# Kernel tuning notes

Measured on AMD Instinct MI355X. Metric: run time of the kernel, lower is better.

The kernel has to match this reference:

```python
import jax, jax.numpy as jnp
from jax import lax
import numpy as np

B, T, F, H, L = 256, 512, 64, 128, 2


def lstm_layer(x, W_ih, W_hh, b_ih, b_hh):
    """PyTorch-style LSTM layer. x:[B,T,I]; W_ih:[4H,I]; W_hh:[4H,H]. Gate order i,f,g,o."""
    b = x.shape[0]
    h_dim = W_hh.shape[1]
    # Precompute input contribution for all timesteps: [B,T,4H]
    xg = jnp.einsum('bti,gi->btg', x, W_ih) + b_ih + b_hh

    def step(carry, xg_t):
        h, c = carry
        g = xg_t + h @ W_hh.T  # [B,4H]
        i, f, gg, o = jnp.split(g, 4, axis=-1)
        c = jax.nn.sigmoid(f) * c + jax.nn.sigmoid(i) * jnp.tanh(gg)
        h = jax.nn.sigmoid(o) * jnp.tanh(c)
        return (h, c), h

    h0 = jnp.zeros((b, h_dim), x.dtype)
    c0 = jnp.zeros((b, h_dim), x.dtype)
    (hT, _), hs = lax.scan(step, (h0, c0), jnp.swapaxes(xg, 0, 1))  # hs:[T,B,H]
    return jnp.swapaxes(hs, 0, 1), hT


def setup_inputs() -> dict:
    key = jax.random.key(0)
    ks = iter(jax.random.split(key, 32))
    s = 0.05
    d = {"x": jax.random.normal(next(ks), (B, T, F), jnp.float32)}
    # encoder: layer0 input F, layer1 input H; decoder: both layers input H
    for name, in0 in (("enc", F), ("dec", H)):
        for l in range(L):
            I = in0 if l == 0 else H
            d[f"{name}{l}_Wih"] = jax.random.normal(next(ks), (4 * H, I), jnp.float32) * s
            d[f"{name}{l}_Whh"] = jax.random.normal(next(ks), (4 * H, H), jnp.float32) * s
            d[f"{name}{l}_bih"] = jax.random.normal(next(ks), (4 * H,), jnp.float32) * s
            d[f"{name}{l}_bhh"] = jax.random.normal(next(ks), (4 * H,), jnp.float32) * s
    d["W_out"] = jax.random.normal(next(ks), (F, H), jnp.float32) * s
    d["b_out"] = jnp.zeros((F,), jnp.float32)
    return d


def reference(x,
              enc0_Wih, enc0_Whh, enc0_bih, enc0_bhh,
              enc1_Wih, enc1_Whh, enc1_bih, enc1_bhh,
              dec0_Wih, dec0_Whh, dec0_bih, dec0_bhh,
              dec1_Wih, dec1_Whh, dec1_bih, dec1_bhh,
              W_out, b_out):
    enc = [(enc0_Wih, enc0_Whh, enc0_bih, enc0_bhh),
           (enc1_Wih, enc1_Whh, enc1_bih, enc1_bhh)]
    dec = [(dec0_Wih, dec0_Whh, dec0_bih, dec0_bhh),
           (dec1_Wih, dec1_Whh, dec1_bih, dec1_bhh)]
    # Encoder: stacked LSTM, keep last layer's final hidden state
    h = x
    hT = None
    for p in enc:
        h, hT = lstm_layer(h, *p)
    # Repeat final hidden over sequence
    dec_in = jnp.broadcast_to(hT[:, None, :], (x.shape[0], x.shape[1], hT.shape[-1]))
    # Decoder: stacked LSTM over full output sequence
    d = dec_in
    for p in dec:
        d, _ = lstm_layer(d, *p)
    # Linear projection back to feature space
    return jnp.einsum('bth,fh->btf', d, W_out) + b_out
```

## Files before the change

kernel.cpp:

```cpp
#include <hip/hip_runtime.h>
#include <cstddef>

namespace {

typedef _Float16 half_t;
typedef _Float16 half2_t __attribute__((ext_vector_type(2)));
typedef _Float16 f16x4 __attribute__((ext_vector_type(4)));
typedef _Float16 f16x8 __attribute__((ext_vector_type(8)));
typedef float f32x4 __attribute__((ext_vector_type(4)));

constexpr int NB = 256;
constexpr int NT = 512;
constexpr int NH = 128;
constexpr int NG = 512;

__device__ __forceinline__ float sigm(float x) { return 1.0f / (1.0f + __expf(-x)); }
__device__ __forceinline__ float tanh_(float x) { return 2.0f / (1.0f + __expf(-2.0f * x)) - 1.0f; }
__device__ __forceinline__ float dot4(float4 w, float4 v, float acc) {
  return fmaf(w.x, v.x, fmaf(w.y, v.y, fmaf(w.z, v.z, fmaf(w.w, v.w, acc))));
}
__device__ __forceinline__ float fdot2(half2_t a, half2_t b, float c) {
  return __builtin_amdgcn_fdot2(a, b, c, false);
}
__device__ __forceinline__ void pinv(half2_t& x) { asm volatile("" : "+v"(x)); }

__global__ void cvt_kernel(const float* __restrict__ s, half_t* __restrict__ d, int n4) {
  int i = blockIdx.x * blockDim.x + threadIdx.x;
  if (i < n4) {
    float4 v = reinterpret_cast<const float4*>(s)[i];
    f16x4 hv = {(half_t)v.x, (half_t)v.y, (half_t)v.z, (half_t)v.w};
    reinterpret_cast<f16x4*>(d)[i] = hv;
  }
}

template <int K, bool AF32, bool F32OUT>
__global__ __launch_bounds__(256) void xg_gemm(
    const void* __restrict__ Ap, const float* __restrict__ Bw,
    const float* __restrict__ b0, const float* __restrict__ b1,
    half_t* __restrict__ Ch, float* __restrict__ Cf, int Nstr)
{
  __shared__ __align__(16) half_t Atile[128 * K];
  __shared__ __align__(16) half_t Btile[64 * K];
  const int tid = threadIdx.x;
  const int m0 = blockIdx.x * 128;
  const int n0 = blockIdx.y * 64;
  char* Ab = (char*)Atile;
  char* Bb = (char*)Btile;

  if (AF32) {
    const float* Af = (const float*)Ap;
    for (int idx = tid; idx < 128 * K / 4; idx += 256) {
      int row = idx / (K / 4), o = idx % (K / 4);
      float4 v = *(const float4*)(Af + (size_t)(m0 + row) * K + 4 * o);
      f16x4 hv = {(half_t)v.x, (half_t)v.y, (half_t)v.z, (half_t)v.w};
      int byte = ((row * K + 4 * o) * 2) ^ ((row & 7) << 4);
      *(f16x4*)(Ab + byte) = hv;
    }
  } else {
    const half_t* Ah = (const half_t*)Ap;
    for (int idx = tid; idx < 128 * K / 8; idx += 256) {
      int row = idx / (K / 8), o = idx % (K / 8);
      uint4 v = *(const uint4*)(Ah + (size_t)(m0 + row) * K + 8 * o);
      int byte = ((row * K + 8 * o) * 2) ^ ((row & 7) << 4);
      *(uint4*)(Ab + byte) = v;
    }
  }
  for (int idx = tid; idx < 64 * K / 4; idx += 256) {
    int row = idx / (K / 4), o = idx % (K / 4);
    float4 v = *(const float4*)(Bw + (size_t)(n0 + row) * K + 4 * o);
    f16x4 hv = {(half_t)v.x, (half_t)v.y, (half_t)v.z, (half_t)v.w};
    int byte = ((row * K + 4 * o) * 2) ^ ((row & 7) << 4);
    *(f16x4*)(Bb + byte) = hv;
  }
  __syncthreads();

  const int lane = tid & 63, w = tid >> 6;
  const int r16 = lane & 15, koff = (lane >> 4) * 8;
  f32x4 acc[2][4];
#pragma unroll
  for (int fm = 0; fm < 2; ++fm)
#pragma unroll
    for (int fn = 0; fn < 4; ++fn) acc[fm][fn] = (f32x4){0.f, 0.f, 0.f, 0.f};

#pragma unroll
  for (int ks = 0; ks < K / 32; ++ks) {
    f16x8 a[2], bf[4];
#pragma unroll
    for (int fm = 0; fm < 2; ++fm) {
      int row = w * 32 + fm * 16 + r16;
      int byte = ((row * K + ks * 32 + koff) * 2) ^ ((row & 7) << 4);
      a[fm] = *(const f16x8*)(Ab + byte);
    }
#pragma unroll
    for (int fn = 0; fn < 4; ++fn) {
      int row = fn * 16 + r16;
      int byte = ((row * K + ks * 32 + koff) * 2) ^ ((row & 7) << 4);
      bf[fn] = *(const f16x8*)(Bb + byte);
    }
#pragma unroll
    for (int fm = 0; fm < 2; ++fm)
#pragma unroll
      for (int fn = 0; fn < 4; ++fn)
        acc[fm][fn] = __builtin_amdgcn_mfma_f32_16x16x32_f16(a[fm], bf[fn], acc[fm][fn], 0, 0, 0);
  }

#pragma unroll
  for (int fm = 0; fm < 2; ++fm)
#pragma unroll
    for (int fn = 0; fn < 4; ++fn) {
      int n = n0 + fn * 16 + r16;
      float bb = (b0 ? b0[n] : 0.f) + (b1 ? b1[n] : 0.f);
#pragma unroll
      for (int q = 0; q < 4; ++q) {
        int m = m0 + w * 32 + fm * 16 + (lane >> 4) * 4 + q;
        float val = acc[fm][fn][q] + bb;
        if (F32OUT) Cf[(size_t)m * Nstr + n] = val;
        else        Ch[(size_t)m * Nstr + n] = (half_t)val;
      }
    }
}

template <int MODE>
__global__ __launch_bounds__(512, 2) void rec_kernel(
    const half_t* __restrict__ xg,
    const float* __restrict__ hT_in,
    const float* __restrict__ WihD,
    const float* __restrict__ bih, const float* __restrict__ bhh,
    const half_t* __restrict__ Whh,
    half_t* __restrict__ seq_out,
    float* __restrict__ hT_out)
{
  const int b = blockIdx.x;
  const int tid = threadIdx.x;
  const int j = tid >> 2;
  const int kq = tid & 3;

  __shared__ __align__(16) half_t hbuf[2][4][48];
  __shared__ __align__(16) half_t xgs[2][8][NG];
  __shared__ float xgc[NG];
  __shared__ float hinf[NH];

  half2_t wh[4][16];
#pragma unroll
  for (int gi = 0; gi < 4; ++gi) {
    const half2_t* p = reinterpret_cast<const half2_t*>(Whh + (size_t)(gi * NH + j) * NH + kq * 32);
#pragma unroll
    for (int r = 0; r < 16; ++r) wh[gi][r] = p[r];
  }
#pragma unroll
  for (int gi = 0; gi < 4; ++gi)
#pragma unroll
    for (int r = 0; r < 16; ++r) pinv(wh[gi][r]);

  if (tid < NH) hbuf[0][tid >> 5][tid & 31] = (half_t)0.0f;
  float c = 0.0f;

  if (MODE == 2) {
    if (tid < NH) hinf[tid] = hT_in[(size_t)b * NH + tid];
    __syncthreads();
    float a0 = bih[tid] + bhh[tid], a1 = 0.f, a2 = 0.f, a3 = 0.f;
    const float4* wr = (const float4*)(WihD + (size_t)tid * NH);
    const float4* hv = (const float4*)hinf;
#pragma unroll
    for (int k = 0; k < 8; ++k) {
      a0 = dot4(wr[4 * k + 0], hv[4 * k + 0], a0);
      a1 = dot4(wr[4 * k + 1], hv[4 * k + 1], a1);
      a2 = dot4(wr[4 * k + 2], hv[4 * k + 2], a2);
      a3 = dot4(wr[4 * k + 3], hv[4 * k + 3], a3);
    }
    xgc[tid] = (a0 + a1) + (a2 + a3);
    __syncthreads();
  }

  half_t g[8];
  const half_t* xrow = nullptr;
  if (MODE != 2) {
    xrow = xg + (size_t)b * NT * NG + tid;
#pragma unroll
    for (int s = 0; s < 8; ++s) g[s] = xrow[(size_t)s * NG];
  }

  for (int ch = 0; ch < NT / 8; ++ch) {
    if (MODE != 2) {
#pragma unroll
      for (int s = 0; s < 8; ++s) xgs[ch & 1][s][tid] = g[s];
      if (ch < NT / 8 - 1) {
#pragma unroll
        for (int s = 0; s < 8; ++s) g[s] = xrow[(size_t)((ch + 1) * 8 + s) * NG];
      }
      __syncthreads();
    }

#pragma unroll 1
    for (int tt = 0; tt < 8; ++tt) {
      const int t = ch * 8 + tt;
      const int p = t & 1;

      float a0 = 0.f, a1 = 0.f, a2 = 0.f, a3 = 0.f;
      const f16x8* hv8 = reinterpret_cast<const f16x8*>(&hbuf[p][kq][0]);
#pragma unroll
      for (int r8 = 0; r8 < 4; ++r8) {
        f16x8 h8 = hv8[r8];
        half2_t h0 = {h8[0], h8[1]}, h1 = {h8[2], h8[3]};
        half2_t h2 = {h8[4], h8[5]}, h3 = {h8[6], h8[7]};
        a0 = fdot2(wh[0][4 * r8 + 0], h0, a0); a0 = fdot2(wh[0][4 * r8 + 1], h1, a0);
        a0 = fdot2(wh[0][4 * r8 + 2], h2, a0); a0 = fdot2(wh[0][4 * r8 + 3], h3, a0);
        a1 = fdot2(wh[1][4 * r8 + 0], h0, a1); a1 = fdot2(wh[1][4 * r8 + 1], h1, a1);
        a1 = fdot2(wh[1][4 * r8 + 2], h2, a1); a1 = fdot2(wh[1][4 * r8 + 3], h3, a1);
        a2 = fdot2(wh[2][4 * r8 + 0], h0, a2); a2 = fdot2(wh[2][4 * r8 + 1], h1, a2);
        a2 = fdot2(wh[2][4 * r8 + 2], h2, a2); a2 = fdot2(wh[2][4 * r8 + 3], h3, a2);
        a3 = fdot2(wh[3][4 * r8 + 0], h0, a3); a3 = fdot2(wh[3][4 * r8 + 1], h1, a3);
        a3 = fdot2(wh[3][4 * r8 + 2], h2, a3); a3 = fdot2(wh[3][4 * r8 + 3], h3, a3);
      }
      a0 += __shfl_xor(a0, 1, 4); a0 += __shfl_xor(a0, 2, 4);
      a1 += __shfl_xor(a1, 1, 4); a1 += __shfl_xor(a1, 2, 4);
      a2 += __shfl_xor(a2, 1, 4); a2 += __shfl_xor(a2, 2, 4);
      a3 += __shfl_xor(a3, 1, 4); a3 += __shfl_xor(a3, 2, 4);

      float xi, xf, xgg, xo;
      if (MODE == 2) {
        xi = xgc[j]; xf = xgc[j + 128]; xgg = xgc[j + 256]; xo = xgc[j + 384];
      } else {
        const half_t* xb = &xgs[ch & 1][tt][0];
        xi = (float)xb[j]; xf = (float)xb[j + 128];
        xgg = (float)xb[j + 256]; xo = (float)xb[j + 384];
      }

      const float ig = sigm(a0 + xi);
      const float fg = sigm(a1 + xf);
      const float gg = tanh_(a2 + xgg);
      const float og = sigm(a3 + xo);
      c = fmaf(fg, c, ig * gg);
      const float h = og * tanh_(c);

      if (kq == 0) {
        hbuf[p ^ 1][j >> 5][j & 31] = (half_t)h;
        if (MODE != 1) seq_out[((size_t)b * NT + t) * NH + j] = (half_t)h;
        else if (t == NT - 1) hT_out[(size_t)b * NH + j] = h;
      }
      __syncthreads();
    }
  }
}

}

extern "C" void kernel_launch(void* const* d_in, const int* in_sizes, int n_in,
                              void* d_out, int out_size, void* d_ws, size_t ws_size,
                              hipStream_t stream) {
  (void)in_sizes; (void)n_in; (void)out_size; (void)ws_size;

  const float* x     = (const float*)d_in[0];
  const float* e0Wih = (const float*)d_in[1];
  const float* e0Whh = (const float*)d_in[2];
  const float* e0bih = (const float*)d_in[3];
  const float* e0bhh = (const float*)d_in[4];
  const float* e1Wih = (const float*)d_in[5];
  const float* e1Whh = (const float*)d_in[6];
  const float* e1bih = (const float*)d_in[7];
  const float* e1bhh = (const float*)d_in[8];
  const float* d0Wih = (const float*)d_in[9];
  const float* d0Whh = (const float*)d_in[10];
  const float* d0bih = (const float*)d_in[11];
  const float* d0bhh = (const float*)d_in[12];
  const float* d1Wih = (const float*)d_in[13];
  const float* d1Whh = (const float*)d_in[14];
  const float* d1bih = (const float*)d_in[15];
  const float* d1bhh = (const float*)d_in[16];
  const float* Wout  = (const float*)d_in[17];
  const float* bout  = (const float*)d_in[18];
  float* out = (float*)d_out;

  half_t* whh0 = (half_t*)d_ws;
  half_t* whh1 = whh0 + 512 * 128;
  half_t* whh2 = whh1 + 512 * 128;
  half_t* whh3 = whh2 + 512 * 128;
  half_t* seqA = whh3 + 512 * 128;
  half_t* xgb  = seqA + (size_t)NB * NT * NH;
  float*  hT   = (float*)(xgb + (size_t)NB * NT * NG);

  cvt_kernel<<<64, 256, 0, stream>>>(e0Whh, whh0, 512 * 128 / 4);
  cvt_kernel<<<64, 256, 0, stream>>>(e1Whh, whh1, 512 * 128 / 4);
  cvt_kernel<<<64, 256, 0, stream>>>(d0Whh, whh2, 512 * 128 / 4);
  cvt_kernel<<<64, 256, 0, stream>>>(d1Whh, whh3, 512 * 128 / 4);

  const int M = NB * NT;
  dim3 gX(M / 128, NG / 64), gP(M / 128, 1), blkG(256);
  dim3 gR(NB), blkR(512);

  xg_gemm<64, true, false><<<gX, blkG, 0, stream>>>(x, e0Wih, e0bih, e0bhh, xgb, nullptr, NG);
  rec_kernel<0><<<gR, blkR, 0, stream>>>(xgb, nullptr, nullptr, nullptr, nullptr, whh0, seqA, nullptr);

  xg_gemm<128, false, false><<<gX, blkG, 0, stream>>>(seqA, e1Wih, e1bih, e1bhh, xgb, nullptr, NG);
  rec_kernel<1><<<gR, blkR, 0, stream>>>(xgb, nullptr, nullptr, nullptr, nullptr, whh1, nullptr, hT);

  rec_kernel<2><<<gR, blkR, 0, stream>>>(nullptr, hT, d0Wih, d0bih, d0bhh, whh2, seqA, nullptr);

  xg_gemm<128, false, false><<<gX, blkG, 0, stream>>>(seqA, d1Wih, d1bih, d1bhh, xgb, nullptr, NG);
  rec_kernel<0><<<gR, blkR, 0, stream>>>(xgb, nullptr, nullptr, nullptr, nullptr, whh3, seqA, nullptr);

  xg_gemm<128, false, true><<<gP, blkG, 0, stream>>>(seqA, Wout, bout, nullptr, nullptr, out, 64);
}
```

Before: 1.984 ms.

## Batch 16 sequences per block and compute LSTM recurrence with MFMA

The recurrent kernel now processes 16 batch rows per block (16 blocks instead of 256) and computes h@W_hh^T with 16x16x32 f16 MFMA instructions, with W_hh held in registers as MFMA fragments. The input-gate GEMM writes its output in a time-major, fragment-tiled layout so each lane loads its gate preactivations directly, prefetched two steps ahead. Hidden states are staged in an 8-deep shared-memory ring and flushed to a time-major sequence buffer every 8 steps. The intent is to replace per-row scalar dot2 math and shuffle reductions with matrix instructions, at the cost of using only 16 workgroups on a large GPU and serial per-step latency per block.

Result: slower. 3.575 ms (+80.2%).

```diff
diff --git a/kernel.cpp b/kernel.cpp
--- a/kernel.cpp
+++ b/kernel.cpp
@@ -4,7 +4,6 @@
 namespace {
 
 typedef _Float16 half_t;
-typedef _Float16 half2_t __attribute__((ext_vector_type(2)));
 typedef _Float16 f16x4 __attribute__((ext_vector_type(4)));
 typedef _Float16 f16x8 __attribute__((ext_vector_type(8)));
 typedef float f32x4 __attribute__((ext_vector_type(4)));
@@ -16,13 +15,11 @@
 
 __device__ __forceinline__ float sigm(float x) { return 1.0f / (1.0f + __expf(-x)); }
 __device__ __forceinline__ float tanh_(float x) { return 2.0f / (1.0f + __expf(-2.0f * x)) - 1.0f; }
-__device__ __forceinline__ float dot4(float4 w, float4 v, float acc) {
-  return fmaf(w.x, v.x, fmaf(w.y, v.y, fmaf(w.z, v.z, fmaf(w.w, v.w, acc))));
-}
-__device__ __forceinline__ float fdot2(half2_t a, half2_t b, float c) {
-  return __builtin_amdgcn_fdot2(a, b, c, false);
-}
-__device__ __forceinline__ void pinv(half2_t& x) { asm volatile("" : "+v"(x)); }
+__device__ __forceinline__ void pinv8(f16x8& x) { asm volatile("" : "+v"(x)); }
+
+__device__ __forceinline__ size_t xg_off(int t, int bblk, int w, int fn, int u, int row) {
+  return ((size_t)((t * 16 + bblk) * 8 + w)) * 1024 + (size_t)((fn * 16 + u) * 16 + row);
+}
 
 __global__ void cvt_kernel(const float* __restrict__ s, half_t* __restrict__ d, int n4) {
   int i = blockIdx.x * blockDim.x + threadIdx.x;
@@ -33,11 +30,11 @@
   }
 }
 
-template <int K, bool AF32, bool F32OUT>
+template <int K, int AMAP, int OUT>
 __global__ __launch_bounds__(256) void xg_gemm(
     const void* __restrict__ Ap, const float* __restrict__ Bw,
     const float* __restrict__ b0, const float* __restrict__ b1,
-    half_t* __restrict__ Ch, float* __restrict__ Cf, int Nstr)
+    half_t* __restrict__ Co, float* __restrict__ Cf)
 {
   __shared__ __align__(16) half_t Atile[128 * K];
   __shared__ __align__(16) half_t Btile[64 * K];
@@ -47,11 +44,12 @@
   char* Ab = (char*)Atile;
   char* Bb = (char*)Btile;
 
-  if (AF32) {
+  if (AMAP == 1) {
     const float* Af = (const float*)Ap;
+    const int t_fix = m0 >> 8, b_base = m0 & 255;
     for (int idx = tid; idx < 128 * K / 4; idx += 256) {
       int row = idx / (K / 4), o = idx % (K / 4);
-      float4 v = *(const float4*)(Af + (size_t)(m0 + row) * K + 4 * o);
+      float4 v = *(const float4*)(Af + ((size_t)(b_base + row) * NT + t_fix) * K + 4 * o);
       f16x4 hv = {(half_t)v.x, (half_t)v.y, (half_t)v.z, (half_t)v.w};
       int byte = ((row * K + 4 * o) * 2) ^ ((row & 7) << 4);
       *(f16x4*)(Ab + byte) = hv;
@@ -74,8 +72,8 @@
   }
   __syncthreads();
 
-  const int lane = tid & 63, w = tid >> 6;
-  const int r16 = lane & 15, koff = (lane >> 4) * 8;
+  const int lane = tid & 63, wv = tid >> 6;
+  const int r16 = lane & 15, g4 = lane >> 4, koff = g4 * 8;
   f32x4 acc[2][4];
 #pragma unroll
   for (int fm = 0; fm < 2; ++fm)
@@ -87,7 +85,7 @@
     f16x8 a[2], bf[4];
 #pragma unroll
     for (int fm = 0; fm < 2; ++fm) {
-      int row = w * 32 + fm * 16 + r16;
+      int row = wv * 32 + fm * 16 + r16;
       int byte = ((row * K + ks * 32 + koff) * 2) ^ ((row & 7) << 4);
       a[fm] = *(const f16x8*)(Ab + byte);
     }
@@ -104,142 +102,176 @@
         acc[fm][fn] = __builtin_amdgcn_mfma_f32_16x16x32_f16(a[fm], bf[fn], acc[fm][fn], 0, 0, 0);
   }
 
-#pragma unroll
-  for (int fm = 0; fm < 2; ++fm)
-#pragma unroll
-    for (int fn = 0; fn < 4; ++fn) {
-      int n = n0 + fn * 16 + r16;
-      float bb = (b0 ? b0[n] : 0.f) + (b1 ? b1[n] : 0.f);
-#pragma unroll
-      for (int q = 0; q < 4; ++q) {
-        int m = m0 + w * 32 + fm * 16 + (lane >> 4) * 4 + q;
-        float val = acc[fm][fn][q] + bb;
-        if (F32OUT) Cf[(size_t)m * Nstr + n] = val;
-        else        Ch[(size_t)m * Nstr + n] = (half_t)val;
-      }
-    }
+  if (OUT == 0) {
+    const int t = m0 >> 8;
+#pragma unroll
+    for (int fm = 0; fm < 2; ++fm)
+#pragma unroll
+      for (int fn = 0; fn < 4; ++fn) {
+        const int gate = n0 + fn * 16 + r16;
+        const float bb = b0[gate] + b1[gate];
+        const int b_lo = (m0 & 255) + wv * 32 + fm * 16 + g4 * 4;
+        const int bblk = b_lo >> 4, row = b_lo & 15;
+        const int fnG = gate >> 7, w2 = (gate & 127) >> 4;
+        const size_t off =
+            ((size_t)(t * 16 + bblk) * 8 + w2) * 1024 + (size_t)((fnG * 16 + r16) * 16 + row);
+        f16x4 pk = {(half_t)(acc[fm][fn][0] + bb), (half_t)(acc[fm][fn][1] + bb),
+                    (half_t)(acc[fm][fn][2] + bb), (half_t)(acc[fm][fn][3] + bb)};
+        *(f16x4*)(Co + off) = pk;
+      }
+  } else {
+    const int t = m0 >> 8;
+#pragma unroll
+    for (int fm = 0; fm < 2; ++fm)
+#pragma unroll
+      for (int fn = 0; fn < 4; ++fn) {
+        const int n = n0 + fn * 16 + r16;
+        const float bb = b0[n];
+#pragma unroll
+        for (int q = 0; q < 4; ++q) {
+          const int b = (m0 & 255) + wv * 32 + fm * 16 + g4 * 4 + q;
+          Cf[((size_t)b * NT + t) * 64 + n] = acc[fm][fn][q] + bb;
+        }
+      }
+  }
 }
 
 template <int MODE>
-__global__ __launch_bounds__(512, 2) void rec_kernel(
-    const half_t* __restrict__ xg,
-    const float* __restrict__ hT_in,
-    const float* __restrict__ WihD,
+__global__ __attribute__((amdgpu_flat_work_group_size(512, 512)))
+__attribute__((amdgpu_waves_per_eu(2, 2))) void rec_mfma(
+    const half_t* __restrict__ xgF,
+    const float* __restrict__ hT_in, const float* __restrict__ Wih32,
     const float* __restrict__ bih, const float* __restrict__ bhh,
     const half_t* __restrict__ Whh,
     half_t* __restrict__ seq_out,
     float* __restrict__ hT_out)
 {
-  const int b = blockIdx.x;
   const int tid = threadIdx.x;
-  const int j = tid >> 2;
-  const int kq = tid & 3;
-
-  __shared__ __align__(16) half_t hbuf[2][4][48];
-  __shared__ __align__(16) half_t xgs[2][8][NG];
-  __shared__ float xgc[NG];
-  __shared__ float hinf[NH];
-
-  half2_t wh[4][16];
-#pragma unroll
-  for (int gi = 0; gi < 4; ++gi) {
-    const half2_t* p = reinterpret_cast<const half2_t*>(Whh + (size_t)(gi * NH + j) * NH + kq * 32);
-#pragma unroll
-    for (int r = 0; r < 16; ++r) wh[gi][r] = p[r];
-  }
-#pragma unroll
-  for (int gi = 0; gi < 4; ++gi)
-#pragma unroll
-    for (int r = 0; r < 16; ++r) pinv(wh[gi][r]);
-
-  if (tid < NH) hbuf[0][tid >> 5][tid & 31] = (half_t)0.0f;
-  float c = 0.0f;
-
+  const int w = tid >> 6, lane = tid & 63;
+  const int u = lane & 15, g4 = lane >> 4;
+  const int bblk = blockIdx.x, b0 = bblk * 16;
+
+  __shared__ __align__(16) half_t hist[8][16][136];
+
+  f16x8 wh[4][4];
+#pragma unroll
+  for (int fn = 0; fn < 4; ++fn)
+#pragma unroll
+    for (int ks = 0; ks < 4; ++ks)
+      wh[fn][ks] =
+          *(const f16x8*)(Whh + (size_t)(fn * 128 + w * 16 + u) * NH + ks * 32 + g4 * 8);
+#pragma unroll
+  for (int fn = 0; fn < 4; ++fn)
+#pragma unroll
+    for (int ks = 0; ks < 4; ++ks) pinv8(wh[fn][ks]);
+
+  {
+    int m = tid >> 5, k0 = (tid & 31) * 4;
+    f16x4 z = {(half_t)0.f, (half_t)0.f, (half_t)0.f, (half_t)0.f};
+    *(f16x4*)&hist[7][m][k0] = z;
+  }
+
+  float c[4] = {0.f, 0.f, 0.f, 0.f};
+
+  f32x4 accC[4];
   if (MODE == 2) {
-    if (tid < NH) hinf[tid] = hT_in[(size_t)b * NH + tid];
+    f16x8 ah[4];
+#pragma unroll
+    for (int ks = 0; ks < 4; ++ks) {
+      const float* hp = hT_in + (size_t)(b0 + u) * NH + ks * 32 + g4 * 8;
+      float4 v0 = *(const float4*)hp, v1 = *(const float4*)(hp + 4);
+      f16x8 t8;
+      t8[0] = (half_t)v0.x; t8[1] = (half_t)v0.y; t8[2] = (half_t)v0.z; t8[3] = (half_t)v0.w;
+      t8[4] = (half_t)v1.x; t8[5] = (half_t)v1.y; t8[6] = (half_t)v1.z; t8[7] = (half_t)v1.w;
+      ah[ks] = t8;
+    }
+#pragma unroll
+    for (int fn = 0; fn < 4; ++fn) {
+      const int gate = fn * 128 + w * 16 + u;
+      f32x4 a = {0.f, 0.f, 0.f, 0.f};
+#pragma unroll
+      for (int ks = 0; ks < 4; ++ks) {
+        const float* wp = Wih32 + (size_t)gate * NH + ks * 32 + g4 * 8;
+        float4 v0 = *(const float4*)wp, v1 = *(const float4*)(wp + 4);
+        f16x8 t8;
+        t8[0] = (half_t)v0.x; t8[1] = (half_t)v0.y; t8[2] = (half_t)v0.z; t8[3] = (half_t)v0.w;
+        t8[4] = (half_t)v1.x; t8[5] = (half_t)v1.y; t8[6] = (half_t)v1.z; t8[7] = (half_t)v1.w;
+        a = __builtin_amdgcn_mfma_f32_16x16x32_f16(ah[ks], t8, a, 0, 0, 0);
+      }
+      const float bs = bih[gate] + bhh[gate];
+      a[0] += bs; a[1] += bs; a[2] += bs; a[3] += bs;
+      accC[fn] = a;
+    }
+  }
+
+  f16x4 st0[4], st1[4];
+  if (MODE != 2) {
+#pragma unroll
+    for (int fn = 0; fn < 4; ++fn) {
+      st0[fn] = *(const f16x4*)(xgF + xg_off(0, bblk, w, fn, u, g4 * 4));
+      st1[fn] = *(const f16x4*)(xgF + xg_off(1, bblk, w, fn, u, g4 * 4));
+    }
+  }
+
+  __syncthreads();
+
+  auto step = [&](int t, f16x4 (&st)[4]) {
+    const int rd = (t + 7) & 7, wr = t & 7;
+
+    f32x4 acc[4];
+    if (MODE == 2) {
+#pragma unroll
+      for (int fn = 0; fn < 4; ++fn) acc[fn] = accC[fn];
+    } else {
+#pragma unroll
+      for (int fn = 0; fn < 4; ++fn) {
+        f16x4 s = st[fn];
+        acc[fn] = (f32x4){(float)s[0], (float)s[1], (float)s[2], (float)s[3]};
+      }
+      if (t + 2 < NT) {
+#pragma unroll
+        for (int fn = 0; fn < 4; ++fn)
+          st[fn] = *(const f16x4*)(xgF + xg_off(t + 2, bblk, w, fn, u, g4 * 4));
+      }
+    }
+
+    f16x8 a[4];
+#pragma unroll
+    for (int ks = 0; ks < 4; ++ks)
+      a[ks] = *(const f16x8*)&hist[rd][u][ks * 32 + g4 * 8];
+#pragma unroll
+    for (int fn = 0; fn < 4; ++fn)
+#pragma unroll
+      for (int ks = 0; ks < 4; ++ks)
+        acc[fn] = __builtin_amdgcn_mfma_f32_16x16x32_f16(a[ks], wh[fn][ks], acc[fn], 0, 0, 0);
+
+#pragma unroll
+    for (int q = 0; q < 4; ++q) {
+      const float ig = sigm(acc[0][q]);
+      const float fg = sigm(acc[1][q]);
+      const float gg = tanh_(acc[2][q]);
+      const float og = sigm(acc[3][q]);
+      c[q] = fmaf(fg, c[q], ig * gg);
+      const float h = og * tanh_(c[q]);
+      hist[wr][g4 * 4 + q][w * 16 + u] = (half_t)h;
+      if (MODE == 1 && t == NT - 1)
+        hT_out[(size_t)(b0 + g4 * 4 + q) * NH + w * 16 + u] = h;
+    }
     __syncthreads();
-    float a0 = bih[tid] + bhh[tid], a1 = 0.f, a2 = 0.f, a3 = 0.f;
-    const float4* wr = (const float4*)(WihD + (size_t)tid * NH);
-    const float4* hv = (const float4*)hinf;
-#pragma unroll
-    for (int k = 0; k < 8; ++k) {
-      a0 = dot4(wr[4 * k + 0], hv[4 * k + 0], a0);
-      a1 = dot4(wr[4 * k + 1], hv[4 * k + 1], a1);
-      a2 = dot4(wr[4 * k + 2], hv[4 * k + 2], a2);
-      a3 = dot4(wr[4 * k + 3], hv[4 * k + 3], a3);
-    }
-    xgc[tid] = (a0 + a1) + (a2 + a3);
-    __syncthreads();
-  }
-
-  half_t g[8];
-  const half_t* xrow = nullptr;
-  if (MODE != 2) {
-    xrow = xg + (size_t)b * NT * NG + tid;
-#pragma unroll
-    for (int s = 0; s < 8; ++s) g[s] = xrow[(size_t)s * NG];
-  }
-
-  for (int ch = 0; ch < NT / 8; ++ch) {
-    if (MODE != 2) {
-#pragma unroll
-      for (int s = 0; s < 8; ++s) xgs[ch & 1][s][tid] = g[s];
-      if (ch < NT / 8 - 1) {
-#pragma unroll
-        for (int s = 0; s < 8; ++s) g[s] = xrow[(size_t)((ch + 1) * 8 + s) * NG];
-      }
+
+    if (MODE != 1 && wr == 7) {
+      const int r = tid >> 2, s = r >> 4, m = r & 15, cc = (tid & 3) * 32;
+      const size_t grow = ((size_t)(t - 7 + s) * NB + b0 + m) * NH + cc;
+#pragma unroll
+      for (int i = 0; i < 4; ++i)
+        *(uint4*)(seq_out + grow + i * 8) = *(const uint4*)&hist[s][m][cc + i * 8];
       __syncthreads();
     }
-
-#pragma unroll 1
-    for (int tt = 0; tt < 8; ++tt) {
-      const int t = ch * 8 + tt;
-      const int p = t & 1;
-
-      float a0 = 0.f, a1 = 0.f, a2 = 0.f, a3 = 0.f;
-      const f16x8* hv8 = reinterpret_cast<const f16x8*>(&hbuf[p][kq][0]);
-#pragma unroll
-      for (int r8 = 0; r8 < 4; ++r8) {
-        f16x8 h8 = hv8[r8];
-        half2_t h0 = {h8[0], h8[1]}, h1 = {h8[2], h8[3]};
-        half2_t h2 = {h8[4], h8[5]}, h3 = {h8[6], h8[7]};
-        a0 = fdot2(wh[0][4 * r8 + 0], h0, a0); a0 = fdot2(wh[0][4 * r8 + 1], h1, a0);
-        a0 = fdot2(wh[0][4 * r8 + 2], h2, a0); a0 = fdot2(wh[0][4 * r8 + 3], h3, a0);
-        a1 = fdot2(wh[1][4 * r8 + 0], h0, a1); a1 = fdot2(wh[1][4 * r8 + 1], h1, a1);
-        a1 = fdot2(wh[1][4 * r8 + 2], h2, a1); a1 = fdot2(wh[1][4 * r8 + 3], h3, a1);
-        a2 = fdot2(wh[2][4 * r8 + 0], h0, a2); a2 = fdot2(wh[2][4 * r8 + 1], h1, a2);
-        a2 = fdot2(wh[2][4 * r8 + 2], h2, a2); a2 = fdot2(wh[2][4 * r8 + 3], h3, a2);
-        a3 = fdot2(wh[3][4 * r8 + 0], h0, a3); a3 = fdot2(wh[3][4 * r8 + 1], h1, a3);
-        a3 = fdot2(wh[3][4 * r8 + 2], h2, a3); a3 = fdot2(wh[3][4 * r8 + 3], h3, a3);
-      }
-      a0 += __shfl_xor(a0, 1, 4); a0 += __shfl_xor(a0, 2, 4);
-      a1 += __shfl_xor(a1, 1, 4); a1 += __shfl_xor(a1, 2, 4);
-      a2 += __shfl_xor(a2, 1, 4); a2 += __shfl_xor(a2, 2, 4);
-      a3 += __shfl_xor(a3, 1, 4); a3 += __shfl_xor(a3, 2, 4);
-
-      float xi, xf, xgg, xo;
-      if (MODE == 2) {
-        xi = xgc[j]; xf = xgc[j + 128]; xgg = xgc[j + 256]; xo = xgc[j + 384];
-      } else {
-        const half_t* xb = &xgs[ch & 1][tt][0];
-        xi = (float)xb[j]; xf = (float)xb[j + 128];
-        xgg = (float)xb[j + 256]; xo = (float)xb[j + 384];
-      }
-
-      const float ig = sigm(a0 + xi);
-      const float fg = sigm(a1 + xf);
-      const float gg = tanh_(a2 + xgg);
-      const float og = sigm(a3 + xo);
-      c = fmaf(fg, c, ig * gg);
-      const float h = og * tanh_(c);
-
-      if (kq == 0) {
-        hbuf[p ^ 1][j >> 5][j & 31] = (half_t)h;
-        if (MODE != 1) seq_out[((size_t)b * NT + t) * NH + j] = (half_t)h;
-        else if (t == NT - 1) hT_out[(size_t)b * NH + j] = h;
-      }
-      __syncthreads();
-    }
+  };
+
+  for (int t2 = 0; t2 < NT; t2 += 2) {
+    step(t2, st0);
+    step(t2 + 1, st1);
   }
 }
 
@@ -276,28 +308,27 @@
   half_t* whh2 = whh1 + 512 * 128;
   half_t* whh3 = whh2 + 512 * 128;
   half_t* seqA = whh3 + 512 * 128;
-  half_t* xgb  = seqA + (size_t)NB * NT * NH;
-  float*  hT   = (float*)(xgb + (size_t)NB * NT * NG);
+  half_t* xgF  = seqA + (size_t)NT * NB * NH;
+  float*  hT   = (float*)(xgF + (size_t)NT * NB * NG);
 
   cvt_kernel<<<64, 256, 0, stream>>>(e0Whh, whh0, 512 * 128 / 4);
   cvt_kernel<<<64, 256, 0, stream>>>(e1Whh, whh1, 512 * 128 / 4);
   cvt_kernel<<<64, 256, 0, stream>>>(d0Whh, whh2, 512 * 128 / 4);
   cvt_kernel<<<64, 256, 0, stream>>>(d1Whh, whh3, 512 * 128 / 4);
 
-  const int M = NB * NT;
-  dim3 gX(M / 128, NG / 64), gP(M / 128, 1), blkG(256);
-  dim3 gR(NB), blkR(512);
-
-  xg_gemm<64, true, false><<<gX, blkG, 0, stream>>>(x, e0Wih, e0bih, e0bhh, xgb, nullptr, NG);
-  rec_kernel<0><<<gR, blkR, 0, stream>>>(xgb, nullptr, nullptr, nullptr, nullptr, whh0, seqA, nullptr);
-
-  xg_gemm<128, false, false><<<gX, blkG, 0, stream>>>(seqA, e1Wih, e1bih, e1bhh, xgb, nullptr, NG);
-  rec_kernel<1><<<gR, blkR, 0, stream>>>(xgb, nullptr, nullptr, nullptr, nullptr, whh1, nullptr, hT);
-
-  rec_kernel<2><<<gR, blkR, 0, stream>>>(nullptr, hT, d0Wih, d0bih, d0bhh, whh2, seqA, nullptr);
-
-  xg_gemm<128, false, false><<<gX, blkG, 0, stream>>>(seqA, d1Wih, d1bih, d1bhh, xgb, nullptr, NG);
-  rec_kernel<0><<<gR, blkR, 0, stream>>>(xgb, nullptr, nullptr, nullptr, nullptr, whh3, seqA, nullptr);
-
-  xg_gemm<128, false, true><<<gP, blkG, 0, stream>>>(seqA, Wout, bout, nullptr, nullptr, out, 64);
-}
+  dim3 blkG(256), gX(NB * NT / 128, NG / 64), gP(NB * NT / 128, 1);
+  dim3 gR(16), blkR(512);
+
+  xg_gemm<64, 1, 0><<<gX, blkG, 0, stream>>>(x, e0Wih, e0bih, e0bhh, xgF, nullptr);
+  rec_mfma<0><<<gR, blkR, 0, stream>>>(xgF, nullptr, nullptr, nullptr, nullptr, whh0,
+                                       seqA, nullptr);
+  xg_gemm<128, 0, 0><<<gX, blkG, 0, stream>>>(seqA, e1Wih, e1bih, e1bhh, xgF, nullptr);
+  rec_mfma<1><<<gR, blkR, 0, stream>>>(xgF, nullptr, nullptr, nullptr, nullptr, whh1,
+                                       nullptr, hT);
+  rec_mfma<2><<<gR, blkR, 0, stream>>>(nullptr, hT, d0Wih, d0bih, d0bhh, whh2,
+                                       seqA, nullptr);
+  xg_gemm<128, 0, 0><<<gX, blkG, 0, stream>>>(seqA, d1Wih, d1bih, d1bhh, xgF, nullptr);
+  rec_mfma<0><<<gR, blkR, 0, stream>>>(xgF, nullptr, nullptr, nullptr, nullptr, whh3,
+                                       seqA, nullptr);
+  xg_gemm<128, 0, 2><<<gP, blkG, 0, stream>>>(seqA, Wout, bout, nullptr, nullptr, out);
+}
```

## Interleave gate columns in xg and prefetch per-step gate inputs into registers

Applied to the files above, without the earlier changes.

The xg GEMM now writes its half-precision output with the four gates of each hidden unit interleaved, so every recurrent thread can fetch its four gate pre-activations as one 8-byte load. The staged shared-memory xg chunks, with their extra per-chunk barrier, are replaced by a two-step register prefetch from global memory. The recurrent weights are held as f16x8 vectors, and the dot products now use independent partial sums to shorten the dependency chain. The trade-off is a global-memory load on every step's critical path, which relies on the prefetch distance of two steps to hide its latency.

Result: slower. 2.352 ms (+18.5%).

```diff
diff --git a/kernel.cpp b/kernel.cpp
--- a/kernel.cpp
+++ b/kernel.cpp
@@ -22,7 +22,7 @@
 __device__ __forceinline__ float fdot2(half2_t a, half2_t b, float c) {
   return __builtin_amdgcn_fdot2(a, b, c, false);
 }
-__device__ __forceinline__ void pinv(half2_t& x) { asm volatile("" : "+v"(x)); }
+__device__ __forceinline__ void pinv8(f16x8& x) { asm volatile("" : "+v"(x)); }
 
 __global__ void cvt_kernel(const float* __restrict__ s, half_t* __restrict__ d, int n4) {
   int i = blockIdx.x * blockDim.x + threadIdx.x;
@@ -115,13 +115,14 @@
         int m = m0 + w * 32 + fm * 16 + (lane >> 4) * 4 + q;
         float val = acc[fm][fn][q] + bb;
         if (F32OUT) Cf[(size_t)m * Nstr + n] = val;
-        else        Ch[(size_t)m * Nstr + n] = (half_t)val;
+        else        Ch[(size_t)m * NG + ((n & 127) << 2) + (n >> 7)] = (half_t)val;
       }
     }
 }
 
 template <int MODE>
-__global__ __launch_bounds__(512, 2) void rec_kernel(
+__global__ __attribute__((amdgpu_flat_work_group_size(512, 512)))
+__attribute__((amdgpu_waves_per_eu(2, 2))) void rec_kernel(
     const half_t* __restrict__ xg,
     const float* __restrict__ hT_in,
     const float* __restrict__ WihD,
@@ -136,25 +137,25 @@
   const int kq = tid & 3;
 
   __shared__ __align__(16) half_t hbuf[2][4][48];
-  __shared__ __align__(16) half_t xgs[2][8][NG];
   __shared__ float xgc[NG];
   __shared__ float hinf[NH];
 
-  half2_t wh[4][16];
+  f16x8 wh8[4][4];
 #pragma unroll
   for (int gi = 0; gi < 4; ++gi) {
-    const half2_t* p = reinterpret_cast<const half2_t*>(Whh + (size_t)(gi * NH + j) * NH + kq * 32);
-#pragma unroll
-    for (int r = 0; r < 16; ++r) wh[gi][r] = p[r];
+    const f16x8* p = reinterpret_cast<const f16x8*>(Whh + (size_t)(gi * NH + j) * NH + kq * 32);
+#pragma unroll
+    for (int r = 0; r < 4; ++r) wh8[gi][r] = p[r];
   }
 #pragma unroll
   for (int gi = 0; gi < 4; ++gi)
 #pragma unroll
-    for (int r = 0; r < 16; ++r) pinv(wh[gi][r]);
+    for (int r = 0; r < 4; ++r) pinv8(wh8[gi][r]);
 
   if (tid < NH) hbuf[0][tid >> 5][tid & 31] = (half_t)0.0f;
   float c = 0.0f;
 
+  float cxi = 0.f, cxf = 0.f, cxg = 0.f, cxo = 0.f;
   if (MODE == 2) {
     if (tid < NH) hinf[tid] = hT_in[(size_t)b * NH + tid];
     __syncthreads();
@@ -170,76 +171,86 @@
     }
     xgc[tid] = (a0 + a1) + (a2 + a3);
     __syncthreads();
-  }
-
-  half_t g[8];
-  const half_t* xrow = nullptr;
+    cxi = xgc[j]; cxf = xgc[j + 128]; cxg = xgc[j + 256]; cxo = xgc[j + 384];
+  }
+
+  const half_t* xbase = nullptr;
+  f16x4 xqA = {}, xqB = {};
   if (MODE != 2) {
-    xrow = xg + (size_t)b * NT * NG + tid;
-#pragma unroll
-    for (int s = 0; s < 8; ++s) g[s] = xrow[(size_t)s * NG];
-  }
-
-  for (int ch = 0; ch < NT / 8; ++ch) {
-    if (MODE != 2) {
-#pragma unroll
-      for (int s = 0; s < 8; ++s) xgs[ch & 1][s][tid] = g[s];
-      if (ch < NT / 8 - 1) {
-#pragma unroll
-        for (int s = 0; s < 8; ++s) g[s] = xrow[(size_t)((ch + 1) * 8 + s) * NG];
+    xbase = xg + ((size_t)b * NT) * NG + (j << 2);
+    xqA = *(const f16x4*)(xbase);
+    xqB = *(const f16x4*)(xbase + NG);
+  }
+
+  __syncthreads();
+
+  auto stepf = [&](int t, int p, f16x4& xq) {
+    f16x4 cur = xq;
+    if (MODE != 2 && t + 2 < NT)
+      xq = *(const f16x4*)(xbase + (size_t)(t + 2) * NG);
+
+    const f16x8* hv8 = reinterpret_cast<const f16x8*>(&hbuf[p][kq][0]);
+
+    float pp[4][4];
+#pragma unroll
+    for (int gi = 0; gi < 4; ++gi)
+#pragma unroll
+      for (int r = 0; r < 4; ++r) pp[gi][r] = 0.f;
+#pragma unroll
+    for (int r8 = 0; r8 < 4; ++r8) {
+      const f16x8 H = hv8[r8];
+      const half2_t h0 = __builtin_shufflevector(H, H, 0, 1);
+      const half2_t h1 = __builtin_shufflevector(H, H, 2, 3);
+      const half2_t h2 = __builtin_shufflevector(H, H, 4, 5);
+      const half2_t h3 = __builtin_shufflevector(H, H, 6, 7);
+#pragma unroll
+      for (int gi = 0; gi < 4; ++gi) {
+        const f16x8 W = wh8[gi][r8];
+        float s = pp[gi][r8];
+        s = fdot2(__builtin_shufflevector(W, W, 0, 1), h0, s);
+        s = fdot2(__builtin_shufflevector(W, W, 2, 3), h1, s);
+        s = fdot2(__builtin_shufflevector(W, W, 4, 5), h2, s);
+        s = fdot2(__builtin_shufflevector(W, W, 6, 7), h3, s);
+        pp[gi][r8] = s;
       }
-      __syncthreads();
-    }
+    }
+    float a0 = (pp[0][0] + pp[0][1]) + (pp[0][2] + pp[0][3]);
+    float a1 = (pp[1][0] + pp[1][1]) + (pp[1][2] + pp[1][3]);
+    float a2 = (pp[2][0] + pp[2][1]) + (pp[2][2] + pp[2][3]);
+    float a3 = (pp[3][0] + pp[3][1]) + (pp[3][2] + pp[3][3]);
+
+    a0 += __shfl_xor(a0, 1, 4); a0 += __shfl_xor(a0, 2, 4);
+    a1 += __shfl_xor(a1, 1, 4); a1 += __shfl_xor(a1, 2, 4);
+    a2 += __shfl_xor(a2, 1, 4); a2 += __shfl_xor(a2, 2, 4);
+    a3 += __shfl_xor(a3, 1, 4); a3 += __shfl_xor(a3, 2, 4);
+
+    float xi, xf, xgg, xo;
+    if (MODE == 2) {
+      xi = cxi; xf = cxf; xgg = cxg; xo = cxo;
+    } else {
+      xi = (float)cur[0]; xf = (float)cur[1];
+      xgg = (float)cur[2]; xo = (float)cur[3];
+    }
+
+    const float ig = sigm(a0 + xi);
+    const float fg = sigm(a1 + xf);
+    const float gg = tanh_(a2 + xgg);
+    const float og = sigm(a3 + xo);
+    c = fmaf(fg, c, ig * gg);
+    const float h = og * tanh_(c);
+
+    if (kq == 0) {
+      hbuf[p ^ 1][j >> 5][j & 31] = (half_t)h;
+      if (MODE != 1) seq_out[((size_t)b * NT + t) * NH + j] = (half_t)h;
+      else if (t == NT - 1) hT_out[(size_t)b * NH + j] = h;
+    }
+    __syncthreads();
+  };
 
 #pragma unroll 1
-    for (int tt = 0; tt < 8; ++tt) {
-      const int t = ch * 8 + tt;
-      const int p = t & 1;
-
-      float a0 = 0.f, a1 = 0.f, a2 = 0.f, a3 = 0.f;
-      const f16x8* hv8 = reinterpret_cast<const f16x8*>(&hbuf[p][kq][0]);
-#pragma unroll
-      for (int r8 = 0; r8 < 4; ++r8) {
-        f16x8 h8 = hv8[r8];
-        half2_t h0 = {h8[0], h8[1]}, h1 = {h8[2], h8[3]};
-        half2_t h2 = {h8[4], h8[5]}, h3 = {h8[6], h8[7]};
-        a0 = fdot2(wh[0][4 * r8 + 0], h0, a0); a0 = fdot2(wh[0][4 * r8 + 1], h1, a0);
-        a0 = fdot2(wh[0][4 * r8 + 2], h2, a0); a0 = fdot2(wh[0][4 * r8 + 3], h3, a0);
-        a1 = fdot2(wh[1][4 * r8 + 0], h0, a1); a1 = fdot2(wh[1][4 * r8 + 1], h1, a1);
-        a1 = fdot2(wh[1][4 * r8 + 2], h2, a1); a1 = fdot2(wh[1][4 * r8 + 3], h3, a1);
-        a2 = fdot2(wh[2][4 * r8 + 0], h0, a2); a2 = fdot2(wh[2][4 * r8 + 1], h1, a2);
-        a2 = fdot2(wh[2][4 * r8 + 2], h2, a2); a2 = fdot2(wh[2][4 * r8 + 3], h3, a2);
-        a3 = fdot2(wh[3][4 * r8 + 0], h0, a3); a3 = fdot2(wh[3][4 * r8 + 1], h1, a3);
-        a3 = fdot2(wh[3][4 * r8 + 2], h2, a3); a3 = fdot2(wh[3][4 * r8 + 3], h3, a3);
-      }
-      a0 += __shfl_xor(a0, 1, 4); a0 += __shfl_xor(a0, 2, 4);
-      a1 += __shfl_xor(a1, 1, 4); a1 += __shfl_xor(a1, 2, 4);
-      a2 += __shfl_xor(a2, 1, 4); a2 += __shfl_xor(a2, 2, 4);
-      a3 += __shfl_xor(a3, 1, 4); a3 += __shfl_xor(a3, 2, 4);
-
-      float xi, xf, xgg, xo;
-      if (MODE == 2) {
-        xi = xgc[j]; xf = xgc[j + 128]; xgg = xgc[j + 256]; xo = xgc[j + 384];
-      } else {
-        const half_t* xb = &xgs[ch & 1][tt][0];
-        xi = (float)xb[j]; xf = (float)xb[j + 128];
-        xgg = (float)xb[j + 256]; xo = (float)xb[j + 384];
-      }
-
-      const float ig = sigm(a0 + xi);
-      const float fg = sigm(a1 + xf);
-      const float gg = tanh_(a2 + xgg);
-      const float og = sigm(a3 + xo);
-      c = fmaf(fg, c, ig * gg);
-      const float h = og * tanh_(c);
-
-      if (kq == 0) {
-        hbuf[p ^ 1][j >> 5][j & 31] = (half_t)h;
-        if (MODE != 1) seq_out[((size_t)b * NT + t) * NH + j] = (half_t)h;
-        else if (t == NT - 1) hT_out[(size_t)b * NH + j] = h;
-      }
-      __syncthreads();
-    }
+  for (int t = 0; t < NT; t += 2) {
+    stepf(t, 0, xqA);
+    stepf(t + 1, 1, xqB);
   }
 }
 
```
